# Kernel tuning notes

Hardware: AMD Instinct MI355X
Metric: run time of the kernel (lower is better)

The kernel has to match this reference:

```python
import jax, jax.numpy as jnp
import numpy as np

B, N, F, H = 2, 2048, 1024, 16
HD = F // H
SQRT_D = float(np.sqrt(F))  # note: module scales by sqrt(in_c), not sqrt(head_dim)


def setup_inputs() -> dict:
    key = jax.random.key(0)
    ks = jax.random.split(key, 9)
    s = 1.0 / np.sqrt(F)
    mk = lambda k: jax.random.uniform(k, (F, F), jnp.float32, -s, s)
    mb = lambda k: jax.random.uniform(k, (F,), jnp.float32, -s, s)
    return {
        "x": jax.random.normal(ks[0], (B, N, F), jnp.float32),
        "Wq": mk(ks[1]), "bq": mb(ks[2]),
        "Wk": mk(ks[3]), "bk": mb(ks[4]),
        "Wv": mk(ks[5]), "bv": mb(ks[6]),
        "Wo": mk(ks[7]), "bo": mb(ks[8]),
    }


def reference(x, Wq, bq, Wk, bk, Wv, bv, Wo, bo):
    b, n, f = x.shape
    # projections (torch Linear: x @ W.T + b); view to (b, n, h, hd)
    q = (x @ Wq.T + bq).reshape(b, n, H, HD)
    k = (x @ Wk.T + bk).reshape(b, n, H, HD)
    v = (x @ Wv.T + bv).reshape(b, n, H, HD)
    score = jnp.einsum('bihd,bjhd->bhij', q, k)
    attn = jax.nn.softmax(score / SQRT_D, axis=-1)
    o = jnp.einsum('bhij,bjhd->bihd', attn, v).reshape(b, n, f)
    return o @ Wo.T + bo
```

## Files before the change

kernel.cpp:

```cpp
#include <hip/hip_runtime.h>
#include <hip/hip_bf16.h>
#include <stdint.h>
#include <stddef.h>

typedef __bf16 bf16;
typedef __attribute__((ext_vector_type(8))) __bf16 bf16x8;
typedef __attribute__((ext_vector_type(4))) __bf16 bf16x4;
typedef __attribute__((ext_vector_type(2))) __bf16 bf16x2;
typedef __attribute__((ext_vector_type(4))) float f32x4;

#define MFMA16(a, b, c) __builtin_amdgcn_mfma_f32_16x16x32_bf16(a, b, c, 0, 0, 0)

#define BB 2
#define SEQ 2048
#define FDIM 1024
#define NH 16
#define HD 64
#define M_TOK 4096
#define N_QKV 3072

#define CSC 0.04508422f

__device__ __forceinline__ void gll16(const bf16* g, bf16* l) {
    __builtin_amdgcn_global_load_lds(
        (const __attribute__((address_space(1))) void*)g,
        (__attribute__((address_space(3))) void*)l, 16, 0, 0);
}

__device__ __forceinline__ bf16 pack_bf16(float f) {
    uint32_t u = __builtin_bit_cast(uint32_t, f);
    uint16_t h = (uint16_t)((u + 0x8000u) >> 16);
    return __builtin_bit_cast(bf16, h);
}

__device__ __forceinline__ uint32_t pk2(float a, float b) {
#if __has_builtin(__builtin_amdgcn_cvt_pk_bf16_f32)
    bf16x2 t = __builtin_amdgcn_cvt_pk_bf16_f32(a, b);
    return __builtin_bit_cast(uint32_t, t);
#else
    uint32_t ua = __builtin_bit_cast(uint32_t, a) + 0x8000u;
    uint32_t ub = __builtin_bit_cast(uint32_t, b) + 0x8000u;
    return __builtin_amdgcn_perm(ub, ua, 0x07060302);
#endif
}

__global__ __launch_bounds__(256) void convert_k(
    const float* __restrict__ x,
    const float* __restrict__ Wq, const float* __restrict__ bq,
    const float* __restrict__ Wk, const float* __restrict__ bk,
    const float* __restrict__ Wv, const float* __restrict__ bv,
    const float* __restrict__ Wo,
    bf16* __restrict__ xb, bf16* __restrict__ Wcat, bf16* __restrict__ Wob,
    float* __restrict__ bcat)
{
    const int tid = blockIdx.x * blockDim.x + threadIdx.x;
    const int nt = gridDim.x * blockDim.x;
    const int NX4 = M_TOK * FDIM / 4;
    const int NW4 = FDIM * FDIM / 4;

    for (int i = tid; i < NX4; i += nt) {
        float4 v = ((const float4*)x)[i];
        bf16x4 o; o[0] = (bf16)v.x; o[1] = (bf16)v.y; o[2] = (bf16)v.z; o[3] = (bf16)v.w;
        ((bf16x4*)xb)[i] = o;
    }
    for (int i = tid; i < NW4; i += nt) {
        float4 v = ((const float4*)Wq)[i];
        bf16x4 o;
        o[0] = (bf16)(v.x * CSC); o[1] = (bf16)(v.y * CSC);
        o[2] = (bf16)(v.z * CSC); o[3] = (bf16)(v.w * CSC);
        ((bf16x4*)Wcat)[i] = o;
        v = ((const float4*)Wk)[i];
        o[0] = (bf16)v.x; o[1] = (bf16)v.y; o[2] = (bf16)v.z; o[3] = (bf16)v.w;
        ((bf16x4*)Wcat)[NW4 + i] = o;
        v = ((const float4*)Wv)[i];
        o[0] = (bf16)v.x; o[1] = (bf16)v.y; o[2] = (bf16)v.z; o[3] = (bf16)v.w;
        ((bf16x4*)Wcat)[2 * NW4 + i] = o;
        v = ((const float4*)Wo)[i];
        o[0] = (bf16)v.x; o[1] = (bf16)v.y; o[2] = (bf16)v.z; o[3] = (bf16)v.w;
        ((bf16x4*)Wob)[i] = o;
    }
    for (int i = tid; i < FDIM; i += nt) {
        bcat[i] = bq[i] * CSC;
        bcat[FDIM + i] = bk[i];
        bcat[2 * FDIM + i] = bv[i];
    }
}

__global__ __launch_bounds__(256) void gemm_bt(
    const bf16* __restrict__ A,
    const bf16* __restrict__ Bw,
    const float* __restrict__ bias,
    bf16* __restrict__ Cb,
    float* __restrict__ Cf,
    bf16* __restrict__ VtOut,
    int M, int N, int K)
{
    __shared__ __align__(16) bf16 As[2][128 * 32];
    __shared__ __align__(16) bf16 Bs[2][128 * 32];

    const int tid = threadIdx.x;
    const int lane = tid & 63;
    const int wave = tid >> 6;
    const int m0 = blockIdx.y * 128;
    const int n0 = blockIdx.x * 128;
    const int wm = (wave >> 1) * 64;
    const int wn = (wave & 1) * 64;
    const int lrow = lane & 15;
    const int lk8 = (lane >> 4) * 8;

    f32x4 acc[4][4] = {};

    const int srow = wave * 16 + (lane >> 2);
    const int scol = (lane & 3) * 8;
    const bf16* Ag = A + (size_t)(m0 + srow) * K + scol;
    const bf16* Bg = Bw + (size_t)(n0 + srow) * K + scol;
    const int wo = (wave * 16) * 32;

    gll16(Ag, &As[0][wo]);
    gll16(Ag + (size_t)64 * K, &As[0][wo + 2048]);
    gll16(Bg, &Bs[0][wo]);
    gll16(Bg + (size_t)64 * K, &Bs[0][wo + 2048]);

    for (int k0 = 0, it = 0; k0 < K; k0 += 32, ++it) {
        const int cur = it & 1;
        __syncthreads();

        if (k0 + 32 < K) {
            const int nxt = cur ^ 1;
            gll16(Ag + k0 + 32, &As[nxt][wo]);
            gll16(Ag + (size_t)64 * K + k0 + 32, &As[nxt][wo + 2048]);
            gll16(Bg + k0 + 32, &Bs[nxt][wo]);
            gll16(Bg + (size_t)64 * K + k0 + 32, &Bs[nxt][wo + 2048]);
        }

        bf16x8 af[4], bfr[4];
#pragma unroll
        for (int s = 0; s < 4; ++s) {
            af[s] = *(const bf16x8*)&As[cur][(wm + s * 16 + lrow) * 32 + lk8];
            bfr[s] = *(const bf16x8*)&Bs[cur][(wn + s * 16 + lrow) * 32 + lk8];
        }
#pragma unroll
        for (int i = 0; i < 4; ++i)
#pragma unroll
            for (int j = 0; j < 4; ++j)
                acc[i][j] = MFMA16(af[i], bfr[j], acc[i][j]);
    }

    const int r0 = (lane >> 4) * 4;
    if (VtOut && n0 >= 2048) {
        const int bql = (m0 >> 11);
#pragma unroll
        for (int i = 0; i < 4; ++i) {
#pragma unroll
            for (int j = 0; j < 4; ++j) {
                const int col = n0 + wn + j * 16 + lrow;
                const float bsv = bias[col];
                const int vh = col - 2048;
                const int row = m0 + wm + i * 16 + r0;
                const int jj = row & (SEQ - 1);
                const int g = jj & 63;
                const int jj2 = (jj & ~63) | ((g >> 5) << 5)
                              | (((g >> 2) & 3) << 3) | (((g >> 4) & 1) << 2);
                bf16x4 vv;
#pragma unroll
                for (int r = 0; r < 4; ++r)
                    vv[r] = pack_bf16(acc[i][j][r] + bsv);
                *(bf16x4*)&VtOut[((size_t)bql * 16 * 64 + vh) * SEQ + jj2] = vv;
            }
        }
        return;
    }
#pragma unroll
    for (int i = 0; i < 4; ++i) {
#pragma unroll
        for (int j = 0; j < 4; ++j) {
            const int col = n0 + wn + j * 16 + lrow;
            const float bsv = bias[col];
#pragma unroll
            for (int r = 0; r < 4; ++r) {
                const int row = m0 + wm + i * 16 + r0 + r;
                const float v = acc[i][j][r] + bsv;
                if (Cb) Cb[(size_t)row * N + col] = pack_bf16(v);
                else    Cf[(size_t)row * N + col] = v;
            }
        }
    }
}

__global__ __launch_bounds__(256) void attn_k(
    const bf16* __restrict__ QKV,
    const bf16* __restrict__ Vt,
    bf16* __restrict__ O)
{
    const int bh = blockIdx.y;
    const int b = bh >> 4;
    const int h = bh & 15;
    const int lane = threadIdx.x & 63;
    const int wave = threadIdx.x >> 6;
    const int lrow = lane & 15;
    const int quad = lane >> 4;
    const int lk8 = quad * 8;

    __shared__ __align__(16) bf16 Ks[2][2][64 * 32];
    __shared__ __align__(16) bf16 Vs[2][2][64 * 32];

    const size_t base = (size_t)b * SEQ * N_QKV;
    const bf16* Qp = QKV + base + h * HD;
    const bf16* Kp = QKV + base + FDIM + h * HD;
    const bf16* Vtp = Vt + (size_t)bh * HD * SEQ;

    const int qr0 = blockIdx.x * 128 + wave * 32;

    bf16x8 qf[2][2];
#pragma unroll
    for (int qt = 0; qt < 2; ++qt)
#pragma unroll
        for (int ks = 0; ks < 2; ++ks)
            qf[qt][ks] = *(const bf16x8*)(Qp + (size_t)(qr0 + qt * 16 + lrow) * N_QKV
                                          + ks * 32 + lk8);

    bf16x8 ones8;
#pragma unroll
    for (int e = 0; e < 8; ++e) ones8[e] = (bf16)1.0f;

    const f32x4 zf = {0.f, 0.f, 0.f, 0.f};

    f32x4 o[2][4] = {};
    f32x4 o4[2] = {};

    const int srow = wave * 16 + (lane >> 2);
    const int scol = (lane & 3) * 8;
    const bf16* kg = Kp + (size_t)srow * N_QKV + scol;
    const bf16* vg = Vtp + (size_t)srow * SEQ + scol;
    const int wo = (wave * 16) * 32;

    gll16(kg, &Ks[0][0][wo]);
    gll16(kg + 32, &Ks[0][1][wo]);
    gll16(vg, &Vs[0][0][wo]);
    gll16(vg + 32, &Vs[0][1][wo]);
    kg += (size_t)64 * N_QKV;
    vg += 64;

    for (int jt = 0; jt < SEQ / 64; ++jt) {
        const int cur = jt & 1;
        __syncthreads();

        if (jt + 1 < SEQ / 64) {
            gll16(kg, &Ks[cur ^ 1][0][wo]);
            gll16(kg + 32, &Ks[cur ^ 1][1][wo]);
            gll16(vg, &Vs[cur ^ 1][0][wo]);
            gll16(vg + 32, &Vs[cur ^ 1][1][wo]);
            kg += (size_t)64 * N_QKV;
            vg += 64;
        }

        f32x4 Sp[4][2];
#pragma unroll
        for (int jn = 0; jn < 4; ++jn) {
            bf16x8 kb0 = *(const bf16x8*)&Ks[cur][0][(jn * 16 + lrow) * 32 + lk8];
            bf16x8 kb1 = *(const bf16x8*)&Ks[cur][1][(jn * 16 + lrow) * 32 + lk8];
            Sp[jn][0] = MFMA16(kb0, qf[0][0], zf);
            Sp[jn][0] = MFMA16(kb1, qf[0][1], Sp[jn][0]);
            Sp[jn][1] = MFMA16(kb0, qf[1][0], zf);
            Sp[jn][1] = MFMA16(kb1, qf[1][1], Sp[jn][1]);
        }

#pragma unroll
        for (int p = 0; p < 2; ++p) {
            union { bf16x8 v; uint32_t d[4]; } pb[2];
#pragma unroll
            for (int qt = 0; qt < 2; ++qt) {
                const f32x4 s0 = Sp[2 * p][qt];
                const f32x4 s1 = Sp[2 * p + 1][qt];
                pb[qt].d[0] = pk2(__builtin_amdgcn_exp2f(s0[0]),
                                  __builtin_amdgcn_exp2f(s0[1]));
                pb[qt].d[1] = pk2(__builtin_amdgcn_exp2f(s0[2]),
                                  __builtin_amdgcn_exp2f(s0[3]));
                pb[qt].d[2] = pk2(__builtin_amdgcn_exp2f(s1[0]),
                                  __builtin_amdgcn_exp2f(s1[1]));
                pb[qt].d[3] = pk2(__builtin_amdgcn_exp2f(s1[2]),
                                  __builtin_amdgcn_exp2f(s1[3]));
            }

            o4[0] = MFMA16(ones8, pb[0].v, o4[0]);
            o4[1] = MFMA16(ones8, pb[1].v, o4[1]);
#pragma unroll
            for (int df = 0; df < 4; ++df) {
                bf16x8 vA = *(const bf16x8*)&Vs[cur][p][(df * 16 + lrow) * 32 + lk8];
                o[0][df] = MFMA16(vA, pb[0].v, o[0][df]);
                o[1][df] = MFMA16(vA, pb[1].v, o[1][df]);
            }
        }
    }

#pragma unroll
    for (int qt = 0; qt < 2; ++qt) {
        const float inv = 1.0f / o4[qt][0];
        const int q = qr0 + qt * 16 + lrow;
#pragma unroll
        for (int df = 0; df < 4; ++df) {
            bf16x4 vv;
#pragma unroll
            for (int r = 0; r < 4; ++r)
                vv[r] = pack_bf16(o[qt][df][r] * inv);
            *(bf16x4*)&O[(size_t)(b * SEQ + q) * FDIM + h * HD + df * 16 + quad * 4] = vv;
        }
    }
}

extern "C" void kernel_launch(void* const* d_in, const int* in_sizes, int n_in,
                              void* d_out, int out_size, void* d_ws, size_t ws_size,
                              hipStream_t stream) {
    (void)in_sizes; (void)n_in; (void)out_size; (void)ws_size;
    const float* x  = (const float*)d_in[0];
    const float* Wq = (const float*)d_in[1];
    const float* bq = (const float*)d_in[2];
    const float* Wk = (const float*)d_in[3];
    const float* bk = (const float*)d_in[4];
    const float* Wv = (const float*)d_in[5];
    const float* bv = (const float*)d_in[6];
    const float* Wo = (const float*)d_in[7];
    const float* bo = (const float*)d_in[8];
    float* out = (float*)d_out;

    char* ws = (char*)d_ws;
    bf16* xb    = (bf16*)(ws);
    bf16* Wcat  = (bf16*)(ws + 8388608);
    bf16* Wob   = (bf16*)(ws + 14680064);
    float* bcat = (float*)(ws + 16777216);
    bf16* QKV   = (bf16*)(ws + 16789504);
    bf16* Vt    = (bf16*)(ws + 41955328);
    bf16* Ob    = xb;

    convert_k<<<dim3(1024), dim3(256), 0, stream>>>(x, Wq, bq, Wk, bk, Wv, bv, Wo,
                                                    xb, Wcat, Wob, bcat);
    gemm_bt<<<dim3(N_QKV / 128, M_TOK / 128), dim3(256), 0, stream>>>(
        xb, Wcat, bcat, QKV, nullptr, Vt, M_TOK, N_QKV, FDIM);
    attn_k<<<dim3(SEQ / 128, BB * NH), dim3(256), 0, stream>>>(QKV, Vt, Ob);
    gemm_bt<<<dim3(FDIM / 128, M_TOK / 128), dim3(256), 0, stream>>>(
        Ob, Wob, bo, nullptr, out, nullptr, M_TOK, FDIM, FDIM);
}
```

Measured before the change: 204.6 us.

## Enlarge attention KV tile, remap blocks to heads, use 64-row tiles for output GEMM

The attention kernel now stages 128 keys per iteration instead of 64, halving the number of barriers and loop iterations, and uses a flattened 1D grid whose block index maps neighbouring blocks to different heads. The output projection GEMM is templated to use 64-row M tiles, giving 512 blocks instead of 256 for better CU occupancy on a 256-CU part. The cost is doubled LDS per attention block, which may lower occupancy, and smaller per-block reuse in the output GEMM.

```diff
diff --git a/kernel.cpp b/kernel.cpp
--- a/kernel.cpp
+++ b/kernel.cpp
@@ -86,6 +86,7 @@
     }
 }
 
+template<int MT>
 __global__ __launch_bounds__(256) void gemm_bt(
     const bf16* __restrict__ A,
     const bf16* __restrict__ Bw,
@@ -95,20 +96,21 @@
     bf16* __restrict__ VtOut,
     int M, int N, int K)
 {
-    __shared__ __align__(16) bf16 As[2][128 * 32];
+    constexpr int RI = MT / 32;
+    __shared__ __align__(16) bf16 As[2][MT * 32];
     __shared__ __align__(16) bf16 Bs[2][128 * 32];
 
     const int tid = threadIdx.x;
     const int lane = tid & 63;
     const int wave = tid >> 6;
-    const int m0 = blockIdx.y * 128;
+    const int m0 = blockIdx.y * MT;
     const int n0 = blockIdx.x * 128;
-    const int wm = (wave >> 1) * 64;
+    const int wm = (wave >> 1) * (MT / 2);
     const int wn = (wave & 1) * 64;
     const int lrow = lane & 15;
     const int lk8 = (lane >> 4) * 8;
 
-    f32x4 acc[4][4] = {};
+    f32x4 acc[RI][4] = {};
 
     const int srow = wave * 16 + (lane >> 2);
     const int scol = (lane & 3) * 8;
@@ -117,7 +119,7 @@
     const int wo = (wave * 16) * 32;
 
     gll16(Ag, &As[0][wo]);
-    gll16(Ag + (size_t)64 * K, &As[0][wo + 2048]);
+    if (MT == 128) gll16(Ag + (size_t)64 * K, &As[0][wo + 2048]);
     gll16(Bg, &Bs[0][wo]);
     gll16(Bg + (size_t)64 * K, &Bs[0][wo + 2048]);
 
@@ -128,29 +130,30 @@
         if (k0 + 32 < K) {
             const int nxt = cur ^ 1;
             gll16(Ag + k0 + 32, &As[nxt][wo]);
-            gll16(Ag + (size_t)64 * K + k0 + 32, &As[nxt][wo + 2048]);
+            if (MT == 128) gll16(Ag + (size_t)64 * K + k0 + 32, &As[nxt][wo + 2048]);
             gll16(Bg + k0 + 32, &Bs[nxt][wo]);
             gll16(Bg + (size_t)64 * K + k0 + 32, &Bs[nxt][wo + 2048]);
         }
 
-        bf16x8 af[4], bfr[4];
-#pragma unroll
-        for (int s = 0; s < 4; ++s) {
+        bf16x8 af[RI], bfr[4];
+#pragma unroll
+        for (int s = 0; s < RI; ++s)
             af[s] = *(const bf16x8*)&As[cur][(wm + s * 16 + lrow) * 32 + lk8];
+#pragma unroll
+        for (int s = 0; s < 4; ++s)
             bfr[s] = *(const bf16x8*)&Bs[cur][(wn + s * 16 + lrow) * 32 + lk8];
-        }
-#pragma unroll
-        for (int i = 0; i < 4; ++i)
+#pragma unroll
+        for (int i = 0; i < RI; ++i)
 #pragma unroll
             for (int j = 0; j < 4; ++j)
                 acc[i][j] = MFMA16(af[i], bfr[j], acc[i][j]);
     }
 
     const int r0 = (lane >> 4) * 4;
-    if (VtOut && n0 >= 2048) {
+    if (MT == 128 && VtOut && n0 >= 2048) {
         const int bql = (m0 >> 11);
 #pragma unroll
-        for (int i = 0; i < 4; ++i) {
+        for (int i = 0; i < RI; ++i) {
 #pragma unroll
             for (int j = 0; j < 4; ++j) {
                 const int col = n0 + wn + j * 16 + lrow;
@@ -171,7 +174,7 @@
         return;
     }
 #pragma unroll
-    for (int i = 0; i < 4; ++i) {
+    for (int i = 0; i < RI; ++i) {
 #pragma unroll
         for (int j = 0; j < 4; ++j) {
             const int col = n0 + wn + j * 16 + lrow;
@@ -192,7 +195,9 @@
     const bf16* __restrict__ Vt,
     bf16* __restrict__ O)
 {
-    const int bh = blockIdx.y;
+    const int bx = blockIdx.x;
+    const int bh = (bx & 7) + 8 * ((bx >> 3) & 3);
+    const int qblk = bx >> 5;
     const int b = bh >> 4;
     const int h = bh & 15;
     const int lane = threadIdx.x & 63;
@@ -201,15 +206,15 @@
     const int quad = lane >> 4;
     const int lk8 = quad * 8;
 
-    __shared__ __align__(16) bf16 Ks[2][2][64 * 32];
-    __shared__ __align__(16) bf16 Vs[2][2][64 * 32];
+    __shared__ __align__(16) bf16 Ks[2][2][128 * 32];
+    __shared__ __align__(16) bf16 Vs[2][4][64 * 32];
 
     const size_t base = (size_t)b * SEQ * N_QKV;
     const bf16* Qp = QKV + base + h * HD;
     const bf16* Kp = QKV + base + FDIM + h * HD;
     const bf16* Vtp = Vt + (size_t)bh * HD * SEQ;
 
-    const int qr0 = blockIdx.x * 128 + wave * 32;
+    const int qr0 = qblk * 128 + wave * 32;
 
     bf16x8 qf[2][2];
 #pragma unroll
@@ -236,42 +241,52 @@
 
     gll16(kg, &Ks[0][0][wo]);
     gll16(kg + 32, &Ks[0][1][wo]);
+    gll16(kg + (size_t)64 * N_QKV, &Ks[0][0][wo + 2048]);
+    gll16(kg + (size_t)64 * N_QKV + 32, &Ks[0][1][wo + 2048]);
     gll16(vg, &Vs[0][0][wo]);
     gll16(vg + 32, &Vs[0][1][wo]);
-    kg += (size_t)64 * N_QKV;
-    vg += 64;
-
-    for (int jt = 0; jt < SEQ / 64; ++jt) {
+    gll16(vg + 64, &Vs[0][2][wo]);
+    gll16(vg + 96, &Vs[0][3][wo]);
+    kg += (size_t)128 * N_QKV;
+    vg += 128;
+
+    for (int jt = 0; jt < SEQ / 128; ++jt) {
         const int cur = jt & 1;
         __syncthreads();
 
-        if (jt + 1 < SEQ / 64) {
-            gll16(kg, &Ks[cur ^ 1][0][wo]);
-            gll16(kg + 32, &Ks[cur ^ 1][1][wo]);
-            gll16(vg, &Vs[cur ^ 1][0][wo]);
-            gll16(vg + 32, &Vs[cur ^ 1][1][wo]);
-            kg += (size_t)64 * N_QKV;
-            vg += 64;
-        }
-
-        f32x4 Sp[4][2];
-#pragma unroll
-        for (int jn = 0; jn < 4; ++jn) {
-            bf16x8 kb0 = *(const bf16x8*)&Ks[cur][0][(jn * 16 + lrow) * 32 + lk8];
-            bf16x8 kb1 = *(const bf16x8*)&Ks[cur][1][(jn * 16 + lrow) * 32 + lk8];
-            Sp[jn][0] = MFMA16(kb0, qf[0][0], zf);
-            Sp[jn][0] = MFMA16(kb1, qf[0][1], Sp[jn][0]);
-            Sp[jn][1] = MFMA16(kb0, qf[1][0], zf);
-            Sp[jn][1] = MFMA16(kb1, qf[1][1], Sp[jn][1]);
-        }
-
-#pragma unroll
-        for (int p = 0; p < 2; ++p) {
+        if (jt + 1 < SEQ / 128) {
+            const int nxt = cur ^ 1;
+            gll16(kg, &Ks[nxt][0][wo]);
+            gll16(kg + 32, &Ks[nxt][1][wo]);
+            gll16(kg + (size_t)64 * N_QKV, &Ks[nxt][0][wo + 2048]);
+            gll16(kg + (size_t)64 * N_QKV + 32, &Ks[nxt][1][wo + 2048]);
+            gll16(vg, &Vs[nxt][0][wo]);
+            gll16(vg + 32, &Vs[nxt][1][wo]);
+            gll16(vg + 64, &Vs[nxt][2][wo]);
+            gll16(vg + 96, &Vs[nxt][3][wo]);
+            kg += (size_t)128 * N_QKV;
+            vg += 128;
+        }
+
+#pragma unroll
+        for (int p = 0; p < 4; ++p) {
+            f32x4 Sp[2][2];
+#pragma unroll
+            for (int m = 0; m < 2; ++m) {
+                const int jn = 2 * p + m;
+                bf16x8 kb0 = *(const bf16x8*)&Ks[cur][0][(jn * 16 + lrow) * 32 + lk8];
+                bf16x8 kb1 = *(const bf16x8*)&Ks[cur][1][(jn * 16 + lrow) * 32 + lk8];
+                Sp[m][0] = MFMA16(kb0, qf[0][0], zf);
+                Sp[m][0] = MFMA16(kb1, qf[0][1], Sp[m][0]);
+                Sp[m][1] = MFMA16(kb0, qf[1][0], zf);
+                Sp[m][1] = MFMA16(kb1, qf[1][1], Sp[m][1]);
+            }
+
             union { bf16x8 v; uint32_t d[4]; } pb[2];
 #pragma unroll
             for (int qt = 0; qt < 2; ++qt) {
-                const f32x4 s0 = Sp[2 * p][qt];
-                const f32x4 s1 = Sp[2 * p + 1][qt];
+                const f32x4 s0 = Sp[0][qt];
+                const f32x4 s1 = Sp[1][qt];
                 pb[qt].d[0] = pk2(__builtin_amdgcn_exp2f(s0[0]),
                                   __builtin_amdgcn_exp2f(s0[1]));
                 pb[qt].d[1] = pk2(__builtin_amdgcn_exp2f(s0[2]),
@@ -334,9 +349,9 @@
 
     convert_k<<<dim3(1024), dim3(256), 0, stream>>>(x, Wq, bq, Wk, bk, Wv, bv, Wo,
                                                     xb, Wcat, Wob, bcat);
-    gemm_bt<<<dim3(N_QKV / 128, M_TOK / 128), dim3(256), 0, stream>>>(
+    gemm_bt<128><<<dim3(N_QKV / 128, M_TOK / 128), dim3(256), 0, stream>>>(
         xb, Wcat, bcat, QKV, nullptr, Vt, M_TOK, N_QKV, FDIM);
-    attn_k<<<dim3(SEQ / 128, BB * NH), dim3(256), 0, stream>>>(QKV, Vt, Ob);
-    gemm_bt<<<dim3(FDIM / 128, M_TOK / 128), dim3(256), 0, stream>>>(
+    attn_k<<<dim3((SEQ / 128) * BB * NH), dim3(256), 0, stream>>>(QKV, Vt, Ob);
+    gemm_bt<64><<<dim3(FDIM / 128, M_TOK / 64), dim3(256), 0, stream>>>(
         Ob, Wob, bo, nullptr, out, nullptr, M_TOK, FDIM, FDIM);
 }
```

Result: faster. 191.0 us (-6.6%).
